# Kernel tuning notes

Measured on AMD Instinct MI355X. Metric: run time of the kernel, lower is better.

The kernel has to match this reference:

```python
import jax, jax.numpy as jnp
import numpy as np

K, N = 8192, 8192
GROUP_SIZE = 128
N_GROUPS = N // GROUP_SIZE  # 64
NBITS = 4
B, T = 8, 32


def setup_inputs() -> dict:
    key = jax.random.key(0)
    k_x, k_q, k_s, k_z, k_m1, k_m2, k_b = jax.random.split(key, 7)
    x = jax.random.normal(k_x, (B, T, N), dtype=jnp.float32)
    # int8 quantized weight codes in [0, 2**nbits - 1]
    W_q = jax.random.randint(k_q, (K, N), 0, 2 ** NBITS, dtype=jnp.int32)
    # group-wise scales/zeros, shaped for broadcast against [K, n_groups, group_size]
    scales = jax.random.uniform(k_s, (K, N_GROUPS, 1), dtype=jnp.float32, minval=0.01, maxval=0.1)
    zeros = jax.random.uniform(k_z, (K, N_GROUPS, 1), dtype=jnp.float32, minval=0.0, maxval=2.0 ** NBITS - 1.0)
    # Sinkhorn row/col scaling factors (positive, near 1)
    mu1 = jnp.exp(0.1 * jax.random.normal(k_m1, (N,), dtype=jnp.float32))
    mu2 = jnp.exp(0.1 * jax.random.normal(k_m2, (K,), dtype=jnp.float32))
    bias = jax.random.normal(k_b, (K,), dtype=jnp.float32)
    return {"x": x, "W_q": W_q, "scales": scales, "zeros": zeros,
            "mu1": mu1, "mu2": mu2, "bias": bias}


def reference(x, W_q, scales, zeros, mu1, mu2, bias):
    k, n = W_q.shape
    n_groups = scales.shape[1]
    group_size = n // n_groups
    # group-wise dequant: (Q - zero) * scale, then Sinkhorn row/col rescale
    Q_g = W_q.astype(jnp.float32).reshape(k, n_groups, group_size)
    W_deq = ((Q_g - zeros) * scales).reshape(k, n)
    W_deq = W_deq * mu2[:, None] * mu1[None, :]
    W_deq = W_deq.astype(x.dtype)
    # nn.functional.linear: x @ W^T + b ; x: [B, T, N] -> [B, T, K]
    out = jnp.einsum('btn,kn->btk', x, W_deq) + bias
    return out
```

## Files before the change

kernel.cpp:

```cpp
#include <hip/hip_runtime.h>
#include <hip/hip_bf16.h>

#define M_DIM 256
#define K_DIM 8192
#define N_DIM 8192
#define NGRP  64

#define BN 128
#define BK 32
#define THREADS 512
#define SPLITN 8
#define CHUNK  (N_DIM / SPLITN)
#define NSTEPS (CHUNK / BK)
#define NG     (CHUNK >> 7)

#define ASIZE 16384
#define SL_OFF (3 * ASIZE)
#define LDS_TOTAL (SL_OFF + NG * 128 * 8)

typedef __bf16 bf16x8 __attribute__((ext_vector_type(8)));
typedef __bf16 bf16x4 __attribute__((ext_vector_type(4)));
typedef float  f32x4  __attribute__((ext_vector_type(4)));

#define SW(a) ((a) ^ ((((a) >> 7) & 7) << 4))

#define GLOAD_LDS16(g, l) __builtin_amdgcn_global_load_lds( \
    (const __attribute__((address_space(1))) void*)(g),     \
    (__attribute__((address_space(3))) void*)(l), 16, 0, 0)

__global__ __launch_bounds__(256) void prep_xs(const float* __restrict__ x,
                                               const float* __restrict__ mu1,
                                               __bf16* __restrict__ xs) {
    int t  = blockIdx.x * 256 + threadIdx.x;
    int n4 = t & 2047;
    int m  = t >> 11;
    int n  = n4 << 2;
    float4 xv = *(const float4*)(x + (size_t)m * N_DIM + n);
    float4 mv = *(const float4*)(mu1 + n);
    bf16x4 o;
    o[0] = (__bf16)(xv.x * mv.x);
    o[1] = (__bf16)(xv.y * mv.y);
    o[2] = (__bf16)(xv.z * mv.z);
    o[3] = (__bf16)(xv.w * mv.w);
    *(bf16x4*)(xs + (size_t)m * N_DIM + n) = o;
}

__global__ __launch_bounds__(THREADS, 4)
void gemm_q(const __bf16* __restrict__ xs, const int* __restrict__ Wq,
            const float* __restrict__ scales, const float* __restrict__ zeros,
            __bf16* __restrict__ partial) {
    extern __shared__ __align__(1024) char lds[];

    const int b     = blockIdx.x;
    const int split = b & 7;
    const int kidx  = b >> 3;
    const int k0    = kidx * BN;
    const int nbase = split * CHUNK;
    const int gbase = split * NG;

    const int tid  = threadIdx.x;
    const int lane = tid & 63;
    const int w    = tid >> 6;
    const int start = kidx & (NSTEPS - 1);

    float* SL = (float*)(lds + SL_OFF);

    {
        int r = tid >> 2, gq = tid & 3;
#pragma unroll
        for (int gg = 0; gg < (NG >> 2); ++gg) {
            int g = (gg << 2) | gq;
            size_t si = (size_t)(k0 + r) * NGRP + gbase + g;
            float s = scales[si];
            float z = zeros[si];
            float2 v; v.x = s; v.y = -z * s;
            *(float2*)&SL[(size_t)((g << 7) + r) * 2] = v;
        }
    }

    const char* asrc[2];
    int aoff[2];
#pragma unroll
    for (int cc = 0; cc < 2; ++cc) {
        int c   = w * 2 + cc;
        int off = c * 1024 + lane * 16;
        int L   = SW(off);
        aoff[cc] = off;
        asrc[cc] = (const char*)xs + ((size_t)(L >> 6) * N_DIM) * 2 + (L & 63);
    }

    const int browL = w * 16 + (lane & 15);
    const int* bptr0 = Wq + (size_t)(k0 + browL) * N_DIM + (lane >> 4) * 8;

#define ISSUE_A(t)                                                        \
    {                                                                     \
        int s_ = ((t) + start) & (NSTEPS - 1);                            \
        char* bs_ = lds + ((t) % 3) * ASIZE;                              \
        size_t so_ = (size_t)(nbase + s_ * BK) * 2;                       \
        GLOAD_LDS16(asrc[0] + so_, bs_ + aoff[0]);                        \
        GLOAD_LDS16(asrc[1] + so_, bs_ + aoff[1]);                        \
    }
#define LOAD_B(t, q0, q1)                                                 \
    {                                                                     \
        int s_ = ((t) + start) & (NSTEPS - 1);                            \
        const int* p_ = bptr0 + (nbase + s_ * BK);                        \
        q0 = *(const int4*)p_;                                            \
        q1 = *(const int4*)(p_ + 4);                                      \
    }

    f32x4 acc[16];
#pragma unroll
    for (int i = 0; i < 16; ++i)
        acc[i] = (f32x4){0.f, 0.f, 0.f, 0.f};

    int4 qa0, qa1, qb0, qb1;

    LOAD_B(0, qa0, qa1);
    ISSUE_A(0);
    asm volatile("" ::: "memory");
    LOAD_B(1, qb0, qb1);
    ISSUE_A(1);
    asm volatile("s_waitcnt lgkmcnt(0)" ::: "memory");

    float sc = 0.f, zs = 0.f;

#define STEP(it, q0c, q1c)                                                \
    {                                                                     \
        if ((it) < NSTEPS - 1) asm volatile("s_waitcnt vmcnt(4)" ::: "memory"); \
        else                   asm volatile("s_waitcnt vmcnt(0)" ::: "memory"); \
        __builtin_amdgcn_s_barrier();      \
        int scur_ = ((it) + start) & (NSTEPS - 1);                        \
        if ((scur_ & 3) == 0 || (it) == 0) {                              \
            float2 v_ = *(float2*)&SL[(size_t)(((scur_ >> 2) << 7) + browL) * 2]; \
            sc = v_.x; zs = v_.y;                                         \
        }                                                                 \
        bf16x8 bv_;                                                       \
        bv_[0] = (__bf16)((float)q0c.x * sc + zs);                        \
        bv_[1] = (__bf16)((float)q0c.y * sc + zs);                        \
        bv_[2] = (__bf16)((float)q0c.z * sc + zs);                        \
        bv_[3] = (__bf16)((float)q0c.w * sc + zs);                        \
        bv_[4] = (__bf16)((float)q1c.x * sc + zs);                        \
        bv_[5] = (__bf16)((float)q1c.y * sc + zs);                        \
        bv_[6] = (__bf16)((float)q1c.z * sc + zs);                        \
        bv_[7] = (__bf16)((float)q1c.w * sc + zs);                        \
        if ((it) + 2 < NSTEPS) {                                          \
            LOAD_B((it) + 2, q0c, q1c);                                   \
            ISSUE_A((it) + 2);                                            \
        }                                                                 \
        const char* bufA_ = lds + ((it) % 3) * ASIZE;                     \
        _Pragma("unroll")                                                 \
        for (int mi = 0; mi < 16; ++mi) {                                 \
            int la_ = (mi * 16 + (lane & 15)) * 64 + (lane >> 4) * 16;    \
            bf16x8 av_ = *(const bf16x8*)(bufA_ + SW(la_));               \
            acc[mi] = __builtin_amdgcn_mfma_f32_16x16x32_bf16(av_, bv_, acc[mi], 0, 0, 0); \
        }                                                                 \
    }

    for (int it = 0; it < NSTEPS; it += 2) {
        STEP(it,     qa0, qa1);
        STEP(it + 1, qb0, qb1);
    }
#undef STEP
#undef ISSUE_A
#undef LOAD_B

    __bf16* outp = partial + (size_t)split * ((size_t)M_DIM * K_DIM);
    const int gk = k0 + w * 16 + (lane & 15);
#pragma unroll
    for (int mi = 0; mi < 16; ++mi) {
        int gm = mi * 16 + (lane >> 4) * 4;
#pragma unroll
        for (int rix = 0; rix < 4; ++rix)
            outp[(size_t)(gm + rix) * K_DIM + gk] = (__bf16)acc[mi][rix];
    }
}

__global__ __launch_bounds__(256) void reduce_out(const __bf16* __restrict__ partial,
                                                  const float* __restrict__ mu2,
                                                  const float* __restrict__ bias,
                                                  float* __restrict__ out) {
    int t  = blockIdx.x * 256 + threadIdx.x;
    int k4 = t & 2047;
    int m  = t >> 11;
    size_t base = (size_t)m * K_DIM + (size_t)k4 * 4;
    float4 s; s.x = 0.f; s.y = 0.f; s.z = 0.f; s.w = 0.f;
#pragma unroll
    for (int sp = 0; sp < SPLITN; ++sp) {
        bf16x4 p = *(const bf16x4*)(partial + (size_t)sp * ((size_t)M_DIM * K_DIM) + base);
        s.x += (float)p[0]; s.y += (float)p[1]; s.z += (float)p[2]; s.w += (float)p[3];
    }
    float4 m2 = *(const float4*)(mu2 + (size_t)k4 * 4);
    float4 bi = *(const float4*)(bias + (size_t)k4 * 4);
    float4 o;
    o.x = s.x * m2.x + bi.x;
    o.y = s.y * m2.y + bi.y;
    o.z = s.z * m2.z + bi.z;
    o.w = s.w * m2.w + bi.w;
    *(float4*)(out + base) = o;
}

extern "C" void kernel_launch(void* const* d_in, const int* in_sizes, int n_in,
                              void* d_out, int out_size, void* d_ws, size_t ws_size,
                              hipStream_t stream) {
    const float* x      = (const float*)d_in[0];
    const int*   Wq     = (const int*)d_in[1];
    const float* scales = (const float*)d_in[2];
    const float* zeros  = (const float*)d_in[3];
    const float* mu1    = (const float*)d_in[4];
    const float* mu2    = (const float*)d_in[5];
    const float* bias   = (const float*)d_in[6];
    float* out = (float*)d_out;

    __bf16* xs = (__bf16*)d_ws;
    const size_t xs_bytes = (size_t)M_DIM * N_DIM * sizeof(__bf16);
    __bf16* partial = (__bf16*)((char*)d_ws + xs_bytes);

    (void)hipFuncSetAttribute((const void*)gemm_q,
                              hipFuncAttributeMaxDynamicSharedMemorySize,
                              LDS_TOTAL);

    prep_xs<<<2048, 256, 0, stream>>>(x, mu1, xs);
    gemm_q<<<64 * SPLITN, THREADS, LDS_TOTAL, stream>>>(xs, Wq, scales, zeros, partial);
    reduce_out<<<2048, 256, 0, stream>>>(partial, mu2, bias, out);
}
```

Measured before the change: 103.0 us.

## Shrink GEMM tile to 64 rows with 4x4 per-warp MFMA tiles and double buffering

Halves the K-tile per block (BN 128→64) and uses 256 threads, so each wave now computes a 64x64 output sub-tile (4 M-tiles × 4 K-columns), reusing each loaded A fragment across four MFMAs instead of one. The A buffer goes from triple to double buffering with a single barrier per step and prefetch distance one, MFMA sections are raised with s_setprio, and the grid doubles to 1024 blocks. The intent is better register-level reuse, fewer LDS reads per MFMA and more blocks for occupancy. The cost is more registers per thread and a shorter prefetch depth, which could expose memory latency.

```diff
diff --git a/kernel.cpp b/kernel.cpp
--- a/kernel.cpp
+++ b/kernel.cpp
@@ -6,17 +6,17 @@
 #define N_DIM 8192
 #define NGRP  64
 
-#define BN 128
+#define BN 64
 #define BK 32
-#define THREADS 512
+#define THREADS 256
 #define SPLITN 8
 #define CHUNK  (N_DIM / SPLITN)
 #define NSTEPS (CHUNK / BK)
 #define NG     (CHUNK >> 7)
 
 #define ASIZE 16384
-#define SL_OFF (3 * ASIZE)
-#define LDS_TOTAL (SL_OFF + NG * 128 * 8)
+#define SL_OFF (2 * ASIZE)
+#define LDS_TOTAL (SL_OFF + 64 * NG * 8)
 
 typedef __bf16 bf16x8 __attribute__((ext_vector_type(8)));
 typedef __bf16 bf16x4 __attribute__((ext_vector_type(4)));
@@ -65,113 +65,131 @@
 
     float* SL = (float*)(lds + SL_OFF);
 
-    {
-        int r = tid >> 2, gq = tid & 3;
-#pragma unroll
-        for (int gg = 0; gg < (NG >> 2); ++gg) {
-            int g = (gg << 2) | gq;
-            size_t si = (size_t)(k0 + r) * NGRP + gbase + g;
-            float s = scales[si];
-            float z = zeros[si];
-            float2 v; v.x = s; v.y = -z * s;
-            *(float2*)&SL[(size_t)((g << 7) + r) * 2] = v;
-        }
-    }
-
-    const char* asrc[2];
-    int aoff[2];
-#pragma unroll
-    for (int cc = 0; cc < 2; ++cc) {
-        int c   = w * 2 + cc;
-        int off = c * 1024 + lane * 16;
+    for (int e = tid; e < 64 * NG; e += THREADS) {
+        int r = e & 63, g = e >> 6;
+        size_t si = (size_t)(k0 + r) * NGRP + gbase + g;
+        float s = scales[si];
+        float z = zeros[si];
+        float2 v; v.x = s; v.y = -z * s;
+        *(float2*)&SL[(size_t)(g * 64 + r) * 2] = v;
+    }
+    asm volatile("s_waitcnt vmcnt(0) lgkmcnt(0)" ::: "memory");
+    __builtin_amdgcn_s_barrier();
+
+    const char* asrc[4];
+    int aoff[4];
+#pragma unroll
+    for (int cc = 0; cc < 4; ++cc) {
+        int off = cc * 4096 + tid * 16;
         int L   = SW(off);
         aoff[cc] = off;
         asrc[cc] = (const char*)xs + ((size_t)(L >> 6) * N_DIM) * 2 + (L & 63);
     }
 
-    const int browL = w * 16 + (lane & 15);
-    const int* bptr0 = Wq + (size_t)(k0 + browL) * N_DIM + (lane >> 4) * 8;
+    const int* bptr[4];
+#pragma unroll
+    for (int ci = 0; ci < 4; ++ci)
+        bptr[ci] = Wq + (size_t)(k0 + ci * 16 + (lane & 15)) * N_DIM + (lane >> 4) * 8;
+
+    int ra[4];
+#pragma unroll
+    for (int mi = 0; mi < 4; ++mi)
+        ra[mi] = SW((w * 64 + mi * 16 + (lane & 15)) * 64 + (lane >> 4) * 16);
 
 #define ISSUE_A(t)                                                        \
     {                                                                     \
         int s_ = ((t) + start) & (NSTEPS - 1);                            \
-        char* bs_ = lds + ((t) % 3) * ASIZE;                              \
+        char* pb_ = lds + ((t) & 1) * ASIZE;                              \
         size_t so_ = (size_t)(nbase + s_ * BK) * 2;                       \
-        GLOAD_LDS16(asrc[0] + so_, bs_ + aoff[0]);                        \
-        GLOAD_LDS16(asrc[1] + so_, bs_ + aoff[1]);                        \
-    }
-#define LOAD_B(t, q0, q1)                                                 \
+        _Pragma("unroll")                                                 \
+        for (int cc = 0; cc < 4; ++cc)                                    \
+            GLOAD_LDS16(asrc[cc] + so_, pb_ + aoff[cc]);                  \
+    }
+#define LOAD_B(t)                                                         \
     {                                                                     \
         int s_ = ((t) + start) & (NSTEPS - 1);                            \
-        const int* p_ = bptr0 + (nbase + s_ * BK);                        \
-        q0 = *(const int4*)p_;                                            \
-        q1 = *(const int4*)(p_ + 4);                                      \
-    }
-
-    f32x4 acc[16];
-#pragma unroll
-    for (int i = 0; i < 16; ++i)
-        acc[i] = (f32x4){0.f, 0.f, 0.f, 0.f};
-
-    int4 qa0, qa1, qb0, qb1;
-
-    LOAD_B(0, qa0, qa1);
+        const int off_ = nbase + s_ * BK;                                 \
+        _Pragma("unroll")                                                 \
+        for (int ci = 0; ci < 4; ++ci) {                                  \
+            qB[ci][0] = *(const int4*)(bptr[ci] + off_);                  \
+            qB[ci][1] = *(const int4*)(bptr[ci] + off_ + 4);              \
+        }                                                                 \
+    }
+
+    f32x4 acc[4][4];
+#pragma unroll
+    for (int i = 0; i < 4; ++i)
+#pragma unroll
+        for (int j = 0; j < 4; ++j)
+            acc[i][j] = (f32x4){0.f, 0.f, 0.f, 0.f};
+
+    int4 qB[4][2];
+    float sc[4], zs[4];
+
+    LOAD_B(0);
+    asm volatile("" ::: "memory");
     ISSUE_A(0);
-    asm volatile("" ::: "memory");
-    LOAD_B(1, qb0, qb1);
-    ISSUE_A(1);
-    asm volatile("s_waitcnt lgkmcnt(0)" ::: "memory");
-
-    float sc = 0.f, zs = 0.f;
-
-#define STEP(it, q0c, q1c)                                                \
+
+#define STEP(it, W2, DO_NEXT)                                             \
     {                                                                     \
-        if ((it) < NSTEPS - 1) asm volatile("s_waitcnt vmcnt(4)" ::: "memory"); \
-        else                   asm volatile("s_waitcnt vmcnt(0)" ::: "memory"); \
-        __builtin_amdgcn_s_barrier();      \
+        asm volatile("s_waitcnt vmcnt(4)" ::: "memory");                  \
         int scur_ = ((it) + start) & (NSTEPS - 1);                        \
         if ((scur_ & 3) == 0 || (it) == 0) {                              \
-            float2 v_ = *(float2*)&SL[(size_t)(((scur_ >> 2) << 7) + browL) * 2]; \
-            sc = v_.x; zs = v_.y;                                         \
-        }                                                                 \
-        bf16x8 bv_;                                                       \
-        bv_[0] = (__bf16)((float)q0c.x * sc + zs);                        \
-        bv_[1] = (__bf16)((float)q0c.y * sc + zs);                        \
-        bv_[2] = (__bf16)((float)q0c.z * sc + zs);                        \
-        bv_[3] = (__bf16)((float)q0c.w * sc + zs);                        \
-        bv_[4] = (__bf16)((float)q1c.x * sc + zs);                        \
-        bv_[5] = (__bf16)((float)q1c.y * sc + zs);                        \
-        bv_[6] = (__bf16)((float)q1c.z * sc + zs);                        \
-        bv_[7] = (__bf16)((float)q1c.w * sc + zs);                        \
-        if ((it) + 2 < NSTEPS) {                                          \
-            LOAD_B((it) + 2, q0c, q1c);                                   \
-            ISSUE_A((it) + 2);                                            \
-        }                                                                 \
-        const char* bufA_ = lds + ((it) % 3) * ASIZE;                     \
-        _Pragma("unroll")                                                 \
-        for (int mi = 0; mi < 16; ++mi) {                                 \
-            int la_ = (mi * 16 + (lane & 15)) * 64 + (lane >> 4) * 16;    \
-            bf16x8 av_ = *(const bf16x8*)(bufA_ + SW(la_));               \
-            acc[mi] = __builtin_amdgcn_mfma_f32_16x16x32_bf16(av_, bv_, acc[mi], 0, 0, 0); \
-        }                                                                 \
-    }
-
-    for (int it = 0; it < NSTEPS; it += 2) {
-        STEP(it,     qa0, qa1);
-        STEP(it + 1, qb0, qb1);
-    }
+            int g_ = scur_ >> 2;                                          \
+            _Pragma("unroll")                                             \
+            for (int ci = 0; ci < 4; ++ci) {                              \
+                float2 v_ = *(float2*)&SL[(size_t)(g_ * 64 + ci * 16 + (lane & 15)) * 2]; \
+                sc[ci] = v_.x; zs[ci] = v_.y;                             \
+            }                                                             \
+        }                                                                 \
+        bf16x8 bv_[4];                                                    \
+        _Pragma("unroll")                                                 \
+        for (int ci = 0; ci < 4; ++ci) {                                  \
+            bv_[ci][0] = (__bf16)((float)qB[ci][0].x * sc[ci] + zs[ci]);  \
+            bv_[ci][1] = (__bf16)((float)qB[ci][0].y * sc[ci] + zs[ci]);  \
+            bv_[ci][2] = (__bf16)((float)qB[ci][0].z * sc[ci] + zs[ci]);  \
+            bv_[ci][3] = (__bf16)((float)qB[ci][0].w * sc[ci] + zs[ci]);  \
+            bv_[ci][4] = (__bf16)((float)qB[ci][1].x * sc[ci] + zs[ci]);  \
+            bv_[ci][5] = (__bf16)((float)qB[ci][1].y * sc[ci] + zs[ci]);  \
+            bv_[ci][6] = (__bf16)((float)qB[ci][1].z * sc[ci] + zs[ci]);  \
+            bv_[ci][7] = (__bf16)((float)qB[ci][1].w * sc[ci] + zs[ci]);  \
+        }                                                                 \
+        if (DO_NEXT) { LOAD_B((it) + 1); }                                \
+        asm volatile("s_waitcnt vmcnt(" W2 ")" ::: "memory");             \
+        __builtin_amdgcn_s_barrier();                                     \
+        if (DO_NEXT) { ISSUE_A((it) + 1); }                               \
+        const char* pA_ = lds + ((it) & 1) * ASIZE;                       \
+        __builtin_amdgcn_s_setprio(1);                                    \
+        _Pragma("unroll")                                                 \
+        for (int mi = 0; mi < 4; ++mi) {                                  \
+            bf16x8 av_ = *(const bf16x8*)(pA_ + ra[mi]);                  \
+            acc[mi][0] = __builtin_amdgcn_mfma_f32_16x16x32_bf16(av_, bv_[0], acc[mi][0], 0, 0, 0); \
+            acc[mi][1] = __builtin_amdgcn_mfma_f32_16x16x32_bf16(av_, bv_[1], acc[mi][1], 0, 0, 0); \
+            acc[mi][2] = __builtin_amdgcn_mfma_f32_16x16x32_bf16(av_, bv_[2], acc[mi][2], 0, 0, 0); \
+            acc[mi][3] = __builtin_amdgcn_mfma_f32_16x16x32_bf16(av_, bv_[3], acc[mi][3], 0, 0, 0); \
+        }                                                                 \
+        __builtin_amdgcn_s_setprio(0);                                    \
+    }
+
+    for (int it = 0; it < NSTEPS - 1; ++it) {
+        STEP(it, "8", true);
+    }
+    STEP(NSTEPS - 1, "0", false);
 #undef STEP
 #undef ISSUE_A
 #undef LOAD_B
 
     __bf16* outp = partial + (size_t)split * ((size_t)M_DIM * K_DIM);
-    const int gk = k0 + w * 16 + (lane & 15);
-#pragma unroll
-    for (int mi = 0; mi < 16; ++mi) {
-        int gm = mi * 16 + (lane >> 4) * 4;
-#pragma unroll
-        for (int rix = 0; rix < 4; ++rix)
-            outp[(size_t)(gm + rix) * K_DIM + gk] = (__bf16)acc[mi][rix];
+#pragma unroll
+    for (int mi = 0; mi < 4; ++mi) {
+#pragma unroll
+        for (int ci = 0; ci < 4; ++ci) {
+            int gk = k0 + ci * 16 + (lane & 15);
+            int gm = w * 64 + mi * 16 + (lane >> 4) * 4;
+#pragma unroll
+            for (int rix = 0; rix < 4; ++rix)
+                outp[(size_t)(gm + rix) * K_DIM + gk] = (__bf16)acc[mi][ci][rix];
+        }
     }
 }
 
@@ -220,6 +238,6 @@
                               LDS_TOTAL);
 
     prep_xs<<<2048, 256, 0, stream>>>(x, mu1, xs);
-    gemm_q<<<64 * SPLITN, THREADS, LDS_TOTAL, stream>>>(xs, Wq, scales, zeros, partial);
+    gemm_q<<<(K_DIM / BN) * SPLITN, THREADS, LDS_TOTAL, stream>>>(xs, Wq, scales, zeros, partial);
     reduce_out<<<2048, 256, 0, stream>>>(partial, mu2, bias, out);
 }
```

After: 328.0 us. +218.4%, slower.
